# Performance work log

Hardware: AMD Instinct MI355X
Metric: run time of the kernel (lower is better)

## Reference

```python
import jax, jax.numpy as jnp
import numpy as np

B, T, C, H = 4, 2048, 1024, 16
HD = C // H  # head_size = 64


def setup_inputs() -> dict:
    key = jax.random.key(0)
    ks = jax.random.split(key, 8)
    s = 0.02
    return {
        "k": jax.random.normal(ks[0], (B, T, C), jnp.float32),
        "q": jax.random.normal(ks[1], (B, T, C), jnp.float32),
        "v": jax.random.normal(ks[2], (B, T, C), jnp.float32),
        "mask": jnp.ones((B, T, T), dtype=bool),
        "Wk": jax.random.normal(ks[3], (C, C), jnp.float32) * s,
        "bk": jnp.zeros((C,), jnp.float32),
        "Wq": jax.random.normal(ks[4], (C, C), jnp.float32) * s,
        "bq": jnp.zeros((C,), jnp.float32),
        "Wv": jax.random.normal(ks[5], (C, C), jnp.float32) * s,
        "bv": jnp.zeros((C,), jnp.float32),
        "Wo": jax.random.normal(ks[6], (C, C), jnp.float32) * s,
        "bo": jnp.zeros((C,), jnp.float32),
    }


def reference(k, q, v, mask, Wk, bk, Wq, bq, Wv, bv, Wo, bo):
    Bn, Tk, Cn = k.shape
    Tq = q.shape[1]
    hd = Cn // H
    # linear projections
    kp = (k @ Wk + bk).reshape(Bn, Tk, H, hd).transpose(0, 2, 1, 3)  # (B,H,Tk,hd)
    qp = (q @ Wq + bq).reshape(Bn, Tq, H, hd).transpose(0, 2, 1, 3)  # (B,H,Tq,hd)
    vp = (v @ Wv + bv).reshape(Bn, Tk, H, hd).transpose(0, 2, 1, 3)  # (B,H,Tk,hd)
    # scaled scores (B,H,Tq,Tk)
    att = jnp.einsum("bhqd,bhkd->bhqk", qp, kp) * (1.0 / jnp.sqrt(jnp.float32(hd)))
    # combined causal + padding mask
    causal = jnp.tril(jnp.ones((Tq, Tk), dtype=bool))  # (Tq,Tk)
    m = causal[None, None, :, :] & mask[:, None, :, :]  # (B,H|1,Tq,Tk)
    att = jnp.where(m, att, jnp.float32(-1e9))
    att = jax.nn.softmax(att, axis=-1)
    # dropout p=0.0 -> identity
    y = jnp.einsum("bhqk,bhkd->bhqd", att, vp)  # (B,H,Tq,hd)
    y = y.transpose(0, 2, 1, 3).reshape(Bn, Tq, Cn)
    return y @ Wo + bo
```

## Files before the change

### kernel.cpp

```cpp
#include <hip/hip_runtime.h>


#define BATCH 4
#define T_SEQ 2048
#define C_DIM 1024
#define NH 16
#define HD 64

typedef _Float16 f16;
typedef __attribute__((ext_vector_type(4))) _Float16 half4;
typedef __attribute__((ext_vector_type(8))) _Float16 half8;
typedef __attribute__((ext_vector_type(4))) float f32x4;

__device__ inline void gld_lds16(const f16* g, f16* l) {
    __builtin_amdgcn_global_load_lds(
        (const __attribute__((address_space(1))) void*)g,
        (__attribute__((address_space(3))) void*)l, 16, 0, 0);
}

__device__ inline void prep_tile(const float* __restrict__ src, f16* __restrict__ dst)
{
    __shared__ __align__(16) f16 Tl[64][72];
    const int tid = threadIdx.x;
    const int k0 = blockIdx.x * 64, n0 = blockIdx.y * 64;
#pragma unroll
    for (int p = 0; p < 4; ++p) {
        const int kr = p * 16 + (tid >> 4);
        const int nc = (tid & 15) * 4;
        float4 v = *(const float4*)(src + (size_t)(k0 + kr) * C_DIM + n0 + nc);
        Tl[nc + 0][kr] = (f16)v.x;
        Tl[nc + 1][kr] = (f16)v.y;
        Tl[nc + 2][kr] = (f16)v.z;
        Tl[nc + 3][kr] = (f16)v.w;
    }
    __syncthreads();
#pragma unroll
    for (int p = 0; p < 2; ++p) {
        const int nr = p * 32 + (tid >> 3);
        const int kc = (tid & 7) * 8;
        *(half8*)(dst + (size_t)(n0 + nr) * C_DIM + k0 + kc) = *(const half8*)&Tl[nr][kc];
    }
}

__global__ __launch_bounds__(256) void prep_weights(const float* __restrict__ src,
                                                    f16* __restrict__ dst)
{
    prep_tile(src, dst);
}

__global__ __launch_bounds__(256) void prep_weights3(const float* __restrict__ W0,
                                                     const float* __restrict__ W1,
                                                     const float* __restrict__ W2,
                                                     f16* __restrict__ D0,
                                                     f16* __restrict__ D1,
                                                     f16* __restrict__ D2)
{
    const int z = blockIdx.z;
    const float* src = (z == 0) ? W0 : (z == 1) ? W1 : W2;
    f16* dst = (z == 0) ? D0 : (z == 1) ? D1 : D2;
    prep_tile(src, dst);
}


__global__ __launch_bounds__(256) void qkv_gemm(const float* __restrict__ Xq,
                                                const float* __restrict__ Xk,
                                                const float* __restrict__ Xv,
                                                const f16* __restrict__ Wt3,
                                                const float* __restrict__ bqp,
                                                const float* __restrict__ bkp,
                                                const float* __restrict__ bvp,
                                                f16* __restrict__ Qp,
                                                f16* __restrict__ Kp,
                                                f16* __restrict__ Vc)
{
    __shared__ __align__(16) f16 As[2][128 * 40];
    __shared__ __align__(16) f16 Bs[2][128 * 32];

    const int g = blockIdx.x >> 6;
    const float* __restrict__ Xf   = (g == 0) ? Xq : (g == 1) ? Xk : Xv;
    const float* __restrict__ bias = (g == 0) ? bqp : (g == 1) ? bkp : bvp;
    const f16* __restrict__ Wt     = Wt3 + (size_t)g * C_DIM * C_DIM;
    f16* __restrict__ outH         = (g == 0) ? Qp : (g == 1) ? Kp : Vc;

    const int tid  = threadIdx.x;
    const int m0   = (blockIdx.x & 63) * 128;
    const int n0   = blockIdx.y * 128;
    const int lane = tid & 63;
    const int wv   = tid >> 6;
    const int wm   = (wv >> 1) * 64;
    const int wn   = (wv & 1) * 64;
    const int l15  = lane & 15;
    const int quad = lane >> 4;
    const int xg   = (quad ^ ((l15 >> 1) & 3)) << 3;
    const int cSwz = ((lane & 3) ^ ((lane >> 3) & 3)) << 3;
    const int ar   = tid / 8;
    const int ac4  = (tid & 7) * 4;
    const int brow = (wv * 2) * 16 + (lane >> 2);

    f32x4 acc[4][4];
#pragma unroll
    for (int i = 0; i < 4; i++)
#pragma unroll
        for (int j = 0; j < 4; j++) acc[i][j] = (f32x4){0.f, 0.f, 0.f, 0.f};

#pragma unroll
    for (int i = 0; i < 4; i++) {
        float4 v = *(const float4*)(Xf + (size_t)(m0 + ar + i * 32) * C_DIM + ac4);
        half4 h;
        h[0] = (f16)v.x; h[1] = (f16)v.y; h[2] = (f16)v.z; h[3] = (f16)v.w;
        *(half4*)&As[0][(ar + i * 32) * 40 + ac4] = h;
    }
#pragma unroll
    for (int i = 0; i < 2; ++i) {
        const int seg = wv * 2 + i;
        gld_lds16(Wt + (size_t)(n0 + brow + i * 16) * C_DIM + cSwz, &Bs[0][seg * 512]);
    }
    __syncthreads();

    for (int kt = 0; kt < 32; ++kt) {
        const int cur = kt & 1, nxt = cur ^ 1;
        const int kk  = (kt + 1) * 32;

        float4 av[4];
        if (kt < 31) {
#pragma unroll
            for (int i = 0; i < 4; i++)
                av[i] = *(const float4*)(Xf + (size_t)(m0 + ar + i * 32) * C_DIM + kk + ac4);
#pragma unroll
            for (int i = 0; i < 2; ++i) {
                const int seg = wv * 2 + i;
                gld_lds16(Wt + (size_t)(n0 + brow + i * 16) * C_DIM + kk + cSwz,
                          &Bs[nxt][seg * 512]);
            }
        }

        half8 af[4], bf[4];
#pragma unroll
        for (int t = 0; t < 4; t++) af[t] = *(const half8*)&As[cur][(wm + t * 16 + l15) * 40 + quad * 8];
#pragma unroll
        for (int t = 0; t < 4; t++) bf[t] = *(const half8*)&Bs[cur][(wn + t * 16 + l15) * 32 + xg];
#pragma unroll
        for (int tm = 0; tm < 4; tm++)
#pragma unroll
            for (int tn = 0; tn < 4; tn++)
                acc[tm][tn] = __builtin_amdgcn_mfma_f32_16x16x32_f16(af[tm], bf[tn], acc[tm][tn], 0, 0, 0);

        if (kt < 31) {
#pragma unroll
            for (int i = 0; i < 4; i++) {
                half4 h;
                h[0] = (f16)av[i].x; h[1] = (f16)av[i].y;
                h[2] = (f16)av[i].z; h[3] = (f16)av[i].w;
                *(half4*)&As[nxt][(ar + i * 32) * 40 + ac4] = h;
            }
        }
        __syncthreads();
    }

#pragma unroll
    for (int tm = 0; tm < 4; tm++) {
        const int gmb = m0 + wm + tm * 16 + quad * 4;
#pragma unroll
        for (int tn = 0; tn < 4; tn++) {
            const int gn = n0 + wn + tn * 16 + l15;
            const float bv = bias[gn];
            const int h = gn >> 6;
            const int d = gn & 63;
#pragma unroll
            for (int r = 0; r < 4; r++) {
                const int row = gmb + r;
                const float val = acc[tm][tn][r] + bv;
                const int b = row >> 11;
                const int t = row & (T_SEQ - 1);
                const size_t hb = ((size_t)(b * NH + h)) * T_SEQ * HD;
                if (g == 0) {
                    outH[hb + (size_t)t * HD + d] = (f16)(val * 0.18033688f);
                } else if (g == 1) {
                    outH[hb + (size_t)t * HD + ((((d >> 3) + t) & 7) << 3) + (d & 7)] = (f16)val;
                } else {
                    outH[hb + (size_t)(t >> 6) * 4096 + d * 64 +
                         ((((t >> 3) + d) & 7) << 3) + (t & 7)] = (f16)val;
                }
            }
        }
    }
}

__global__ __launch_bounds__(256) void gemm_out(const f16* __restrict__ Xh,
                                                const f16* __restrict__ Wt,
                                                const float* __restrict__ bias,
                                                float* __restrict__ outF)
{
    __shared__ __align__(16) f16 As[2][128 * 32];
    __shared__ __align__(16) f16 Bs[2][128 * 32];

    const int tid  = threadIdx.x;
    const int m0   = blockIdx.x * 128;
    const int n0   = blockIdx.y * 128;
    const int lane = tid & 63;
    const int wv   = tid >> 6;
    const int wm   = (wv >> 1) * 64;
    const int wn   = (wv & 1) * 64;
    const int l15  = lane & 15;
    const int quad = lane >> 4;
    const int xg   = (quad ^ ((l15 >> 1) & 3)) << 3;
    const int cSwz = ((lane & 3) ^ ((lane >> 3) & 3)) << 3;
    const int brow = (wv * 2) * 16 + (lane >> 2);

    f32x4 acc[4][4];
#pragma unroll
    for (int i = 0; i < 4; i++)
#pragma unroll
        for (int j = 0; j < 4; j++) acc[i][j] = (f32x4){0.f, 0.f, 0.f, 0.f};

#pragma unroll
    for (int i = 0; i < 2; ++i) {
        const int seg = wv * 2 + i;
        gld_lds16(Xh + (size_t)(m0 + brow + i * 16) * C_DIM + cSwz, &As[0][seg * 512]);
        gld_lds16(Wt + (size_t)(n0 + brow + i * 16) * C_DIM + cSwz, &Bs[0][seg * 512]);
    }
    __syncthreads();

    for (int kt = 0; kt < 32; ++kt) {
        const int cur = kt & 1, nxt = cur ^ 1;
        const int kk  = (kt + 1) * 32;

        if (kt < 31) {
#pragma unroll
            for (int i = 0; i < 2; ++i) {
                const int seg = wv * 2 + i;
                gld_lds16(Xh + (size_t)(m0 + brow + i * 16) * C_DIM + kk + cSwz, &As[nxt][seg * 512]);
                gld_lds16(Wt + (size_t)(n0 + brow + i * 16) * C_DIM + kk + cSwz, &Bs[nxt][seg * 512]);
            }
        }

        half8 af[4], bf[4];
#pragma unroll
        for (int t = 0; t < 4; t++) af[t] = *(const half8*)&As[cur][(wm + t * 16 + l15) * 32 + xg];
#pragma unroll
        for (int t = 0; t < 4; t++) bf[t] = *(const half8*)&Bs[cur][(wn + t * 16 + l15) * 32 + xg];
#pragma unroll
        for (int tm = 0; tm < 4; tm++)
#pragma unroll
            for (int tn = 0; tn < 4; tn++)
                acc[tm][tn] = __builtin_amdgcn_mfma_f32_16x16x32_f16(af[tm], bf[tn], acc[tm][tn], 0, 0, 0);
        __syncthreads();
    }

#pragma unroll
    for (int tm = 0; tm < 4; tm++) {
        const int gmb = m0 + wm + tm * 16 + quad * 4;
#pragma unroll
        for (int tn = 0; tn < 4; tn++) {
            const int gn = n0 + wn + tn * 16 + l15;
            const float bv = bias[gn];
#pragma unroll
            for (int r = 0; r < 4; r++)
                outF[(size_t)(gmb + r) * C_DIM + gn] = acc[tm][tn][r] + bv;
        }
    }
}

__global__ __launch_bounds__(256) void attn_kernel(const f16* __restrict__ Qp,
                                                   const f16* __restrict__ Kp,
                                                   const f16* __restrict__ Vc,
                                                   f16* __restrict__ Y)
{
    __shared__ __align__(16) f16 Ks[2][4096];
    __shared__ __align__(16) f16 Vs[2][4096];

    const int tid  = threadIdx.x;
    const int lane = tid & 63;
    const int wv   = tid >> 6;
    const int l15  = lane & 15;
    const int quad = lane >> 4;
    const int bh   = blockIdx.x & 63;
    const int ub   = blockIdx.x >> 6;
    const int u    = (ub << 2) | wv;
    int qT[2];
    qT[0] = 16 * u;
    qT[1] = 2032 - 16 * u;

    const f16* Qh = Qp + (size_t)bh * T_SEQ * HD;
    const f16* Kh = Kp + (size_t)bh * T_SEQ * HD;
    const f16* Vh = Vc + (size_t)bh * T_SEQ * HD;

    half8 aq[2][2];
#pragma unroll
    for (int m = 0; m < 2; m++)
#pragma unroll
        for (int kh = 0; kh < 2; kh++)
            aq[m][kh] = *(const half8*)(Qh + (size_t)(qT[m] + l15) * HD + kh * 32 + quad * 8);

    f32x4 o[2][4];
#pragma unroll
    for (int m = 0; m < 2; m++)
#pragma unroll
        for (int dt = 0; dt < 4; dt++) o[m][dt] = (f32x4){0.f, 0.f, 0.f, 0.f};
    float lsum[2] = {0.f, 0.f};

    const int nC0   = (16 * u + 79) >> 6;
    const int nC1   = (2111 - 16 * u) >> 6;
    const int nCblk = (2111 - 64 * ub) >> 6;

    auto stage = [&](int buf, int kc) {
        const f16* kg = Kh + (size_t)kc * 4096 + wv * 512;
        const f16* vg = Vh + (size_t)kc * 4096 + wv * 512;
        f16* kl = &Ks[buf][wv * 512];
        f16* vl = &Vs[buf][wv * 512];
        gld_lds16(kg + lane * 8, kl);
        gld_lds16(kg + 2048 + lane * 8, kl + 2048);
        gld_lds16(vg + lane * 8, vl);
        gld_lds16(vg + 2048 + lane * 8, vl + 2048);
    };

    stage(0, 0);
    __syncthreads();

    for (int kc = 0; kc < nCblk; ++kc) {
        const int cur = kc & 1;
        if (kc + 1 < nCblk) stage(cur ^ 1, kc + 1);

        if (kc < nC1) {
            const int k0 = kc * 64;
            const int mStart = (kc < nC0) ? 0 : 1;

            f32x4 st[2][4];
#pragma unroll
            for (int nt = 0; nt < 4; ++nt) {
                const f16* kr = &Ks[cur][(nt * 16 + l15) * 64];
                half8 bk0 = *(const half8*)(kr + (((quad + l15) & 7) << 3));
                half8 bk1 = *(const half8*)(kr + (((4 + quad + l15) & 7) << 3));
                {
                    f32x4 z = (f32x4){0.f, 0.f, 0.f, 0.f};
                    z = __builtin_amdgcn_mfma_f32_16x16x32_f16(bk0, aq[1][0], z, 0, 0, 0);
                    z = __builtin_amdgcn_mfma_f32_16x16x32_f16(bk1, aq[1][1], z, 0, 0, 0);
                    st[1][nt] = z;
                }
                if (mStart == 0) {
                    f32x4 z = (f32x4){0.f, 0.f, 0.f, 0.f};
                    z = __builtin_amdgcn_mfma_f32_16x16x32_f16(bk0, aq[0][0], z, 0, 0, 0);
                    z = __builtin_amdgcn_mfma_f32_16x16x32_f16(bk1, aq[0][1], z, 0, 0, 0);
                    st[0][nt] = z;
                }
            }

            half4 pf[2][4];
#pragma unroll
            for (int m = 0; m < 2; ++m) {
                if (m < mStart) continue;
                const bool needMask = (k0 + 63 > qT[m]);
                const int q = qT[m] + l15;
#pragma unroll
                for (int nt = 0; nt < 4; ++nt) {
#pragma unroll
                    for (int r = 0; r < 4; ++r) {
                        const int key = k0 + nt * 16 + quad * 4 + r;
                        float p = __builtin_exp2f(st[m][nt][r]);
                        if (needMask && key > q) p = 0.f;
                        lsum[m] += p;
                        pf[m][nt][r] = (f16)p;
                    }
                }
            }

#pragma unroll
            for (int nt = 0; nt < 4; ++nt) {
                const int c0 = nt * 2 + (quad >> 1);
#pragma unroll
                for (int dt = 0; dt < 4; ++dt) {
                    const int d = dt * 16 + l15;
                    half4 bv = *(const half4*)(&Vs[cur][d * 64 + (((c0 + d) & 7) << 3) + ((quad & 1) << 2)]);
                    o[1][dt] = __builtin_amdgcn_mfma_f32_16x16x16f16(pf[1][nt], bv, o[1][dt], 0, 0, 0);
                    if (mStart == 0)
                        o[0][dt] = __builtin_amdgcn_mfma_f32_16x16x16f16(pf[0][nt], bv, o[0][dt], 0, 0, 0);
                }
            }
        }
        __syncthreads();
    }

    const int b = bh >> 4;
    const int h = bh & 15;
#pragma unroll
    for (int m = 0; m < 2; m++) {
        float l = lsum[m];
        l += __shfl_xor(l, 16);
        l += __shfl_xor(l, 32);
#pragma unroll
        for (int r = 0; r < 4; r++) {
            const float lr  = __shfl(l, quad * 4 + r);
            const float inv = 1.0f / lr;
            const int qr = qT[m] + quad * 4 + r;
#pragma unroll
            for (int dt = 0; dt < 4; dt++)
                Y[((size_t)(b * T_SEQ + qr)) * C_DIM + h * HD + dt * 16 + l15] = (f16)(o[m][dt][r] * inv);
        }
    }
}

extern "C" void kernel_launch(void* const* d_in, const int* in_sizes, int n_in,
                              void* d_out, int out_size, void* d_ws, size_t ws_size,
                              hipStream_t stream)
{
    const float* k  = (const float*)d_in[0];
    const float* q  = (const float*)d_in[1];
    const float* v  = (const float*)d_in[2];
    const float* Wk = (const float*)d_in[4];
    const float* bk = (const float*)d_in[5];
    const float* Wq = (const float*)d_in[6];
    const float* bq = (const float*)d_in[7];
    const float* Wv = (const float*)d_in[8];
    const float* bv = (const float*)d_in[9];
    const float* Wo = (const float*)d_in[10];
    const float* bo = (const float*)d_in[11];
    float* out = (float*)d_out;

    const size_t E  = (size_t)BATCH * T_SEQ * C_DIM;
    const size_t WE = (size_t)C_DIM * C_DIM;

    f16* R0 = (f16*)d_ws;
    f16* R1 = R0 + E;
    f16* R2 = R1 + E;
    f16* R3 = R2 + E;

    f16* Kp  = R0;
    f16* Qp  = R1;
    f16* Vc  = R2;
    f16* Y   = R3;
    f16* WtQ = R3;
    f16* WtK = R3 + WE;
    f16* WtV = R3 + 2 * WE;
    f16* WtO = R1;

    dim3 blk(256);
    prep_weights3<<<dim3(16, 16, 3), blk, 0, stream>>>(Wq, Wk, Wv, WtQ, WtK, WtV);
    qkv_gemm<<<dim3(192, 8), blk, 0, stream>>>(q, k, v, WtQ, bq, bk, bv, Qp, Kp, Vc);
    attn_kernel<<<dim3(1024), blk, 0, stream>>>(Qp, Kp, Vc, Y);
    prep_weights<<<dim3(16, 16), blk, 0, stream>>>(Wo, WtO);
    gemm_out<<<dim3(64, 8), blk, 0, stream>>>(Y, WtO, bo, out);
}
```

Measured before the change: 418.3 us.

## Software-pipeline GEMM A-tile loads two steps ahead with explicit waitcnt barriers

Both the QKV projection GEMM and the output projection GEMM now prefetch the A operand into registers two k-steps ahead. The main loop is unrolled by two with ping-pong register buffers, and __syncthreads is replaced by hand-placed s_waitcnt vmcnt/lgkmcnt plus s_barrier and sched_barrier fences. In the output GEMM, the A tile moves from direct global-to-LDS loads to register loads followed by LDS stores. The aim is to hide global load latency behind the MFMA work and avoid waiting on all outstanding memory operations at each barrier. In exchange it adds register pressure and relies on hand-counted vmcnt values being correct.

```diff
diff --git a/kernel.cpp b/kernel.cpp
--- a/kernel.cpp
+++ b/kernel.cpp
@@ -60,7 +60,6 @@
     f16* dst = (z == 0) ? D0 : (z == 1) ? D1 : D2;
     prep_tile(src, dst);
 }
-
 
 __global__ __launch_bounds__(256) void qkv_gemm(const float* __restrict__ Xq,
                                                 const float* __restrict__ Xk,
@@ -111,50 +110,72 @@
         *(half4*)&As[0][(ar + i * 32) * 40 + ac4] = h;
     }
 #pragma unroll
-    for (int i = 0; i < 2; ++i) {
-        const int seg = wv * 2 + i;
-        gld_lds16(Wt + (size_t)(n0 + brow + i * 16) * C_DIM + cSwz, &Bs[0][seg * 512]);
-    }
-    __syncthreads();
-
-    for (int kt = 0; kt < 32; ++kt) {
-        const int cur = kt & 1, nxt = cur ^ 1;
-        const int kk  = (kt + 1) * 32;
-
-        float4 av[4];
-        if (kt < 31) {
-#pragma unroll
-            for (int i = 0; i < 4; i++)
-                av[i] = *(const float4*)(Xf + (size_t)(m0 + ar + i * 32) * C_DIM + kk + ac4);
-#pragma unroll
-            for (int i = 0; i < 2; ++i) {
-                const int seg = wv * 2 + i;
-                gld_lds16(Wt + (size_t)(n0 + brow + i * 16) * C_DIM + kk + cSwz,
-                          &Bs[nxt][seg * 512]);
-            }
-        }
-
+    for (int i = 0; i < 2; ++i)
+        gld_lds16(Wt + (size_t)(n0 + brow + i * 16) * C_DIM + cSwz, &Bs[0][(wv * 2 + i) * 512]);
+    __builtin_amdgcn_sched_barrier(0);
+    float4 avA[4], avB[4];
+#pragma unroll
+    for (int i = 0; i < 4; i++)
+        avA[i] = *(const float4*)(Xf + (size_t)(m0 + ar + i * 32) * C_DIM + 32 + ac4);
+    asm volatile("s_waitcnt vmcnt(4) lgkmcnt(0)" ::: "memory");
+    __builtin_amdgcn_sched_barrier(0);
+    __builtin_amdgcn_s_barrier();
+
+#define QKV_STEP(KT, CUR, NXT, AVC, AVN, VMEND)                                          \
+    {                                                                                    \
+        const int kk1 = ((KT) + 1) * 32;                                                 \
+        _Pragma("unroll")                                                                \
+        for (int i = 0; i < 2; ++i)                                                      \
+            gld_lds16(Wt + (size_t)(n0 + brow + i * 16) * C_DIM + kk1 + cSwz,            \
+                      &Bs[NXT][(wv * 2 + i) * 512]);                                     \
+        __builtin_amdgcn_sched_barrier(0);                           \
+        if ((KT) + 2 < 32) {                                                             \
+            const int kk2 = ((KT) + 2) * 32;                                             \
+            _Pragma("unroll")                                                            \
+            for (int i = 0; i < 4; i++)                                                  \
+                AVN[i] = *(const float4*)(Xf + (size_t)(m0 + ar + i * 32) * C_DIM + kk2 + ac4); \
+        }                                                                                \
+        half8 af[4], bf[4];                                                              \
+        _Pragma("unroll")                                                                \
+        for (int t = 0; t < 4; t++)                                                      \
+            af[t] = *(const half8*)&As[CUR][(wm + t * 16 + l15) * 40 + quad * 8];        \
+        _Pragma("unroll")                                                                \
+        for (int t = 0; t < 4; t++)                                                      \
+            bf[t] = *(const half8*)&Bs[CUR][(wn + t * 16 + l15) * 32 + xg];              \
+        _Pragma("unroll")                                                                \
+        for (int tm = 0; tm < 4; tm++)                                                   \
+            _Pragma("unroll")                                                            \
+            for (int tn = 0; tn < 4; tn++)                                               \
+                acc[tm][tn] = __builtin_amdgcn_mfma_f32_16x16x32_f16(af[tm], bf[tn], acc[tm][tn], 0, 0, 0); \
+        _Pragma("unroll")                                                                \
+        for (int i = 0; i < 4; i++) {                                                    \
+            half4 h;                                                                     \
+            h[0] = (f16)AVC[i].x; h[1] = (f16)AVC[i].y;                                  \
+            h[2] = (f16)AVC[i].z; h[3] = (f16)AVC[i].w;                                  \
+            *(half4*)&As[NXT][(ar + i * 32) * 40 + ac4] = h;                             \
+        }                                                                                \
+        asm volatile("s_waitcnt " VMEND " lgkmcnt(0)" ::: "memory");                     \
+        __builtin_amdgcn_sched_barrier(0);                                               \
+        __builtin_amdgcn_s_barrier();                                                    \
+    }
+
+    for (int kt = 0; kt < 30; kt += 2) {
+        QKV_STEP(kt,     0, 1, avA, avB, "vmcnt(4)");
+        QKV_STEP(kt + 1, 1, 0, avB, avA, "vmcnt(4)");
+    }
+    QKV_STEP(30, 0, 1, avA, avB, "vmcnt(0)");
+#undef QKV_STEP
+    {
         half8 af[4], bf[4];
 #pragma unroll
-        for (int t = 0; t < 4; t++) af[t] = *(const half8*)&As[cur][(wm + t * 16 + l15) * 40 + quad * 8];
-#pragma unroll
-        for (int t = 0; t < 4; t++) bf[t] = *(const half8*)&Bs[cur][(wn + t * 16 + l15) * 32 + xg];
+        for (int t = 0; t < 4; t++) af[t] = *(const half8*)&As[1][(wm + t * 16 + l15) * 40 + quad * 8];
+#pragma unroll
+        for (int t = 0; t < 4; t++) bf[t] = *(const half8*)&Bs[1][(wn + t * 16 + l15) * 32 + xg];
 #pragma unroll
         for (int tm = 0; tm < 4; tm++)
 #pragma unroll
             for (int tn = 0; tn < 4; tn++)
                 acc[tm][tn] = __builtin_amdgcn_mfma_f32_16x16x32_f16(af[tm], bf[tn], acc[tm][tn], 0, 0, 0);
-
-        if (kt < 31) {
-#pragma unroll
-            for (int i = 0; i < 4; i++) {
-                half4 h;
-                h[0] = (f16)av[i].x; h[1] = (f16)av[i].y;
-                h[2] = (f16)av[i].z; h[3] = (f16)av[i].w;
-                *(half4*)&As[nxt][(ar + i * 32) * 40 + ac4] = h;
-            }
-        }
-        __syncthreads();
     }
 
 #pragma unroll
@@ -215,36 +236,69 @@
 
 #pragma unroll
     for (int i = 0; i < 2; ++i) {
-        const int seg = wv * 2 + i;
-        gld_lds16(Xh + (size_t)(m0 + brow + i * 16) * C_DIM + cSwz, &As[0][seg * 512]);
-        gld_lds16(Wt + (size_t)(n0 + brow + i * 16) * C_DIM + cSwz, &Bs[0][seg * 512]);
-    }
-    __syncthreads();
-
-    for (int kt = 0; kt < 32; ++kt) {
-        const int cur = kt & 1, nxt = cur ^ 1;
-        const int kk  = (kt + 1) * 32;
-
-        if (kt < 31) {
-#pragma unroll
-            for (int i = 0; i < 2; ++i) {
-                const int seg = wv * 2 + i;
-                gld_lds16(Xh + (size_t)(m0 + brow + i * 16) * C_DIM + kk + cSwz, &As[nxt][seg * 512]);
-                gld_lds16(Wt + (size_t)(n0 + brow + i * 16) * C_DIM + kk + cSwz, &Bs[nxt][seg * 512]);
-            }
-        }
-
+        gld_lds16(Xh + (size_t)(m0 + brow + i * 16) * C_DIM + cSwz, &As[0][(wv * 2 + i) * 512]);
+        gld_lds16(Wt + (size_t)(n0 + brow + i * 16) * C_DIM + cSwz, &Bs[0][(wv * 2 + i) * 512]);
+    }
+    __builtin_amdgcn_sched_barrier(0);
+    half8 avA[2], avB[2];
+#pragma unroll
+    for (int i = 0; i < 2; ++i)
+        avA[i] = *(const half8*)(Xh + (size_t)(m0 + brow + i * 16) * C_DIM + 32 + cSwz);
+    asm volatile("s_waitcnt vmcnt(2) lgkmcnt(0)" ::: "memory");
+    __builtin_amdgcn_sched_barrier(0);
+    __builtin_amdgcn_s_barrier();
+
+#define OUT_STEP(KT, CUR, NXT, AVC, AVN, VMEND)                                          \
+    {                                                                                    \
+        const int kk1 = ((KT) + 1) * 32;                                                 \
+        _Pragma("unroll")                                                                \
+        for (int i = 0; i < 2; ++i)                                                      \
+            gld_lds16(Wt + (size_t)(n0 + brow + i * 16) * C_DIM + kk1 + cSwz,            \
+                      &Bs[NXT][(wv * 2 + i) * 512]);                                     \
+        __builtin_amdgcn_sched_barrier(0);                                               \
+        if ((KT) + 2 < 32) {                                                             \
+            const int kk2 = ((KT) + 2) * 32;                                             \
+            _Pragma("unroll")                                                            \
+            for (int i = 0; i < 2; ++i)                                                  \
+                AVN[i] = *(const half8*)(Xh + (size_t)(m0 + brow + i * 16) * C_DIM + kk2 + cSwz); \
+        }                                                                                \
+        half8 af[4], bf[4];                                                              \
+        _Pragma("unroll")                                                                \
+        for (int t = 0; t < 4; t++)                                                      \
+            af[t] = *(const half8*)&As[CUR][(wm + t * 16 + l15) * 32 + xg];              \
+        _Pragma("unroll")                                                                \
+        for (int t = 0; t < 4; t++)                                                      \
+            bf[t] = *(const half8*)&Bs[CUR][(wn + t * 16 + l15) * 32 + xg];              \
+        _Pragma("unroll")                                                                \
+        for (int tm = 0; tm < 4; tm++)                                                   \
+            _Pragma("unroll")                                                            \
+            for (int tn = 0; tn < 4; tn++)                                               \
+                acc[tm][tn] = __builtin_amdgcn_mfma_f32_16x16x32_f16(af[tm], bf[tn], acc[tm][tn], 0, 0, 0); \
+        _Pragma("unroll")                                                                \
+        for (int i = 0; i < 2; ++i)                                                      \
+            *(half8*)&As[NXT][(wv * 2 + i) * 512 + lane * 8] = AVC[i];                   \
+        asm volatile("s_waitcnt " VMEND " lgkmcnt(0)" ::: "memory");                     \
+        __builtin_amdgcn_sched_barrier(0);                                               \
+        __builtin_amdgcn_s_barrier();                                                    \
+    }
+
+    for (int kt = 0; kt < 30; kt += 2) {
+        OUT_STEP(kt,     0, 1, avA, avB, "vmcnt(2)");
+        OUT_STEP(kt + 1, 1, 0, avB, avA, "vmcnt(2)");
+    }
+    OUT_STEP(30, 0, 1, avA, avB, "vmcnt(0)");
+#undef OUT_STEP
+    {
         half8 af[4], bf[4];
 #pragma unroll
-        for (int t = 0; t < 4; t++) af[t] = *(const half8*)&As[cur][(wm + t * 16 + l15) * 32 + xg];
-#pragma unroll
-        for (int t = 0; t < 4; t++) bf[t] = *(const half8*)&Bs[cur][(wn + t * 16 + l15) * 32 + xg];
+        for (int t = 0; t < 4; t++) af[t] = *(const half8*)&As[1][(wm + t * 16 + l15) * 32 + xg];
+#pragma unroll
+        for (int t = 0; t < 4; t++) bf[t] = *(const half8*)&Bs[1][(wn + t * 16 + l15) * 32 + xg];
 #pragma unroll
         for (int tm = 0; tm < 4; tm++)
 #pragma unroll
             for (int tn = 0; tn < 4; tn++)
                 acc[tm][tn] = __builtin_amdgcn_mfma_f32_16x16x32_f16(af[tm], bf[tn], acc[tm][tn], 0, 0, 0);
-        __syncthreads();
     }
 
 #pragma unroll
```

Result: slower. 437.0 us (+4.5%).

## Deepen QKV GEMM prefetch to two stages with explicit waitcnt scheduling

Applied to the files above, without the earlier changes.

The QKV projection GEMM now prefetches two k-tiles ahead. The fp32 activations are held in two rotating register sets and the fp16 weights in a triple-buffered LDS ring. The loop is unrolled by two, and __syncthreads is replaced with manual s_waitcnt vmcnt counts, sched_barriers and s_barrier, so global loads stay in flight across iterations. This is meant to hide global-memory latency better, at the cost of more LDS and registers and of fragile hand-counted wait values.

```diff
diff --git a/kernel.cpp b/kernel.cpp
--- a/kernel.cpp
+++ b/kernel.cpp
@@ -60,7 +60,6 @@
     f16* dst = (z == 0) ? D0 : (z == 1) ? D1 : D2;
     prep_tile(src, dst);
 }
-
 
 __global__ __launch_bounds__(256) void qkv_gemm(const float* __restrict__ Xq,
                                                 const float* __restrict__ Xk,
@@ -74,7 +73,7 @@
                                                 f16* __restrict__ Vc)
 {
     __shared__ __align__(16) f16 As[2][128 * 40];
-    __shared__ __align__(16) f16 Bs[2][128 * 32];
+    __shared__ __align__(16) f16 Bs[3][128 * 32];
 
     const int g = blockIdx.x >> 6;
     const float* __restrict__ Xf   = (g == 0) ? Xq : (g == 1) ? Xk : Xv;
@@ -103,58 +102,112 @@
 #pragma unroll
         for (int j = 0; j < 4; j++) acc[i][j] = (f32x4){0.f, 0.f, 0.f, 0.f};
 
+    float4 rA[4], rB[4];
+
+#pragma unroll
+    for (int i = 0; i < 4; i++)
+        rA[i] = *(const float4*)(Xf + (size_t)(m0 + ar + i * 32) * C_DIM + ac4);
+#pragma unroll
+    for (int i = 0; i < 2; ++i)
+        gld_lds16(Wt + (size_t)(n0 + brow + i * 16) * C_DIM + cSwz, &Bs[0][(wv * 2 + i) * 512]);
+#pragma unroll
+    for (int i = 0; i < 4; i++)
+        rB[i] = *(const float4*)(Xf + (size_t)(m0 + ar + i * 32) * C_DIM + 32 + ac4);
+#pragma unroll
+    for (int i = 0; i < 2; ++i)
+        gld_lds16(Wt + (size_t)(n0 + brow + i * 16) * C_DIM + 32 + cSwz, &Bs[1][(wv * 2 + i) * 512]);
+    __builtin_amdgcn_sched_barrier(0);
+    asm volatile("s_waitcnt vmcnt(8)" ::: "memory");
+    __builtin_amdgcn_sched_barrier(0);
 #pragma unroll
     for (int i = 0; i < 4; i++) {
-        float4 v = *(const float4*)(Xf + (size_t)(m0 + ar + i * 32) * C_DIM + ac4);
         half4 h;
-        h[0] = (f16)v.x; h[1] = (f16)v.y; h[2] = (f16)v.z; h[3] = (f16)v.w;
+        h[0] = (f16)rA[i].x; h[1] = (f16)rA[i].y; h[2] = (f16)rA[i].z; h[3] = (f16)rA[i].w;
         *(half4*)&As[0][(ar + i * 32) * 40 + ac4] = h;
     }
-#pragma unroll
-    for (int i = 0; i < 2; ++i) {
-        const int seg = wv * 2 + i;
-        gld_lds16(Wt + (size_t)(n0 + brow + i * 16) * C_DIM + cSwz, &Bs[0][seg * 512]);
-    }
-    __syncthreads();
-
-    for (int kt = 0; kt < 32; ++kt) {
-        const int cur = kt & 1, nxt = cur ^ 1;
-        const int kk  = (kt + 1) * 32;
-
-        float4 av[4];
-        if (kt < 31) {
-#pragma unroll
-            for (int i = 0; i < 4; i++)
-                av[i] = *(const float4*)(Xf + (size_t)(m0 + ar + i * 32) * C_DIM + kk + ac4);
-#pragma unroll
-            for (int i = 0; i < 2; ++i) {
-                const int seg = wv * 2 + i;
-                gld_lds16(Wt + (size_t)(n0 + brow + i * 16) * C_DIM + kk + cSwz,
-                          &Bs[nxt][seg * 512]);
-            }
-        }
-
+    asm volatile("s_waitcnt vmcnt(6) lgkmcnt(0)" ::: "memory");
+    __builtin_amdgcn_sched_barrier(0);
+    __builtin_amdgcn_s_barrier();
+
+#define QKV_STEP(KT, RLOAD, RWRITE)                                                      \
+    {                                                                                    \
+        const int cur = (KT) & 1, nxt = cur ^ 1;                                         \
+        const int bc  = (KT) % 3, bn = ((KT) + 2) % 3;                                   \
+        const int kk2 = ((KT) + 2) * 32;                                                 \
+        _Pragma("unroll")                                                                \
+        for (int i = 0; i < 4; i++)                                                      \
+            RLOAD[i] = *(const float4*)(Xf + (size_t)(m0 + ar + i * 32) * C_DIM + kk2 + ac4); \
+        _Pragma("unroll")                                                                \
+        for (int i = 0; i < 2; ++i)                                                      \
+            gld_lds16(Wt + (size_t)(n0 + brow + i * 16) * C_DIM + kk2 + cSwz,            \
+                      &Bs[bn][(wv * 2 + i) * 512]);                                      \
+        __builtin_amdgcn_sched_barrier(0);                                               \
+        half8 af[4], bf[4];                                                              \
+        _Pragma("unroll")                                                                \
+        for (int t = 0; t < 4; t++)                                                      \
+            af[t] = *(const half8*)&As[cur][(wm + t * 16 + l15) * 40 + quad * 8];        \
+        _Pragma("unroll")                                                                \
+        for (int t = 0; t < 4; t++)                                                      \
+            bf[t] = *(const half8*)&Bs[bc][(wn + t * 16 + l15) * 32 + xg];               \
+        _Pragma("unroll")                                                                \
+        for (int tm = 0; tm < 4; tm++)                                                   \
+            _Pragma("unroll")                                                            \
+            for (int tn = 0; tn < 4; tn++)                                               \
+                acc[tm][tn] = __builtin_amdgcn_mfma_f32_16x16x32_f16(af[tm], bf[tn], acc[tm][tn], 0, 0, 0); \
+        asm volatile("s_waitcnt vmcnt(8)" ::: "memory");               \
+        __builtin_amdgcn_sched_barrier(0);                                               \
+        _Pragma("unroll")                                                                \
+        for (int i = 0; i < 4; i++) {                                                    \
+            half4 h;                                                                     \
+            h[0] = (f16)RWRITE[i].x; h[1] = (f16)RWRITE[i].y;                            \
+            h[2] = (f16)RWRITE[i].z; h[3] = (f16)RWRITE[i].w;                            \
+            *(half4*)&As[nxt][(ar + i * 32) * 40 + ac4] = h;                             \
+        }                                                                                \
+        asm volatile("s_waitcnt vmcnt(6) lgkmcnt(0)" ::: "memory");    \
+        __builtin_amdgcn_sched_barrier(0);                                               \
+        __builtin_amdgcn_s_barrier();                                                    \
+    }
+
+    for (int kt = 0; kt < 30; kt += 2) {
+        QKV_STEP(kt,     rA, rB);
+        QKV_STEP(kt + 1, rB, rA);
+    }
+#undef QKV_STEP
+
+    {
         half8 af[4], bf[4];
 #pragma unroll
-        for (int t = 0; t < 4; t++) af[t] = *(const half8*)&As[cur][(wm + t * 16 + l15) * 40 + quad * 8];
-#pragma unroll
-        for (int t = 0; t < 4; t++) bf[t] = *(const half8*)&Bs[cur][(wn + t * 16 + l15) * 32 + xg];
+        for (int t = 0; t < 4; t++) af[t] = *(const half8*)&As[0][(wm + t * 16 + l15) * 40 + quad * 8];
+#pragma unroll
+        for (int t = 0; t < 4; t++) bf[t] = *(const half8*)&Bs[0][(wn + t * 16 + l15) * 32 + xg];
 #pragma unroll
         for (int tm = 0; tm < 4; tm++)
 #pragma unroll
             for (int tn = 0; tn < 4; tn++)
                 acc[tm][tn] = __builtin_amdgcn_mfma_f32_16x16x32_f16(af[tm], bf[tn], acc[tm][tn], 0, 0, 0);
-
-        if (kt < 31) {
-#pragma unroll
-            for (int i = 0; i < 4; i++) {
-                half4 h;
-                h[0] = (f16)av[i].x; h[1] = (f16)av[i].y;
-                h[2] = (f16)av[i].z; h[3] = (f16)av[i].w;
-                *(half4*)&As[nxt][(ar + i * 32) * 40 + ac4] = h;
-            }
-        }
-        __syncthreads();
+        asm volatile("s_waitcnt vmcnt(2)" ::: "memory");
+        __builtin_amdgcn_sched_barrier(0);
+#pragma unroll
+        for (int i = 0; i < 4; i++) {
+            half4 h;
+            h[0] = (f16)rB[i].x; h[1] = (f16)rB[i].y; h[2] = (f16)rB[i].z; h[3] = (f16)rB[i].w;
+            *(half4*)&As[1][(ar + i * 32) * 40 + ac4] = h;
+        }
+        asm volatile("s_waitcnt vmcnt(0) lgkmcnt(0)" ::: "memory");
+        __builtin_amdgcn_sched_barrier(0);
+        __builtin_amdgcn_s_barrier();
+    }
+    {
+        half8 af[4], bf[4];
+#pragma unroll
+        for (int t = 0; t < 4; t++) af[t] = *(const half8*)&As[1][(wm + t * 16 + l15) * 40 + quad * 8];
+#pragma unroll
+        for (int t = 0; t < 4; t++) bf[t] = *(const half8*)&Bs[1][(wn + t * 16 + l15) * 32 + xg];
+#pragma unroll
+        for (int tm = 0; tm < 4; tm++)
+#pragma unroll
+            for (int tn = 0; tn < 4; tn++)
+                acc[tm][tn] = __builtin_amdgcn_mfma_f32_16x16x32_f16(af[tm], bf[tn], acc[tm][tn], 0, 0, 0);
     }
 
 #pragma unroll
@@ -215,9 +268,8 @@
 
 #pragma unroll
     for (int i = 0; i < 2; ++i) {
-        const int seg = wv * 2 + i;
-        gld_lds16(Xh + (size_t)(m0 + brow + i * 16) * C_DIM + cSwz, &As[0][seg * 512]);
-        gld_lds16(Wt + (size_t)(n0 + brow + i * 16) * C_DIM + cSwz, &Bs[0][seg * 512]);
+        gld_lds16(Xh + (size_t)(m0 + brow + i * 16) * C_DIM + cSwz, &As[0][(wv * 2 + i) * 512]);
+        gld_lds16(Wt + (size_t)(n0 + brow + i * 16) * C_DIM + cSwz, &Bs[0][(wv * 2 + i) * 512]);
     }
     __syncthreads();
 
@@ -228,9 +280,8 @@
         if (kt < 31) {
 #pragma unroll
             for (int i = 0; i < 2; ++i) {
-                const int seg = wv * 2 + i;
-                gld_lds16(Xh + (size_t)(m0 + brow + i * 16) * C_DIM + kk + cSwz, &As[nxt][seg * 512]);
-                gld_lds16(Wt + (size_t)(n0 + brow + i * 16) * C_DIM + kk + cSwz, &Bs[nxt][seg * 512]);
+                gld_lds16(Xh + (size_t)(m0 + brow + i * 16) * C_DIM + kk + cSwz, &As[nxt][(wv * 2 + i) * 512]);
+                gld_lds16(Wt + (size_t)(n0 + brow + i * 16) * C_DIM + kk + cSwz, &Bs[nxt][(wv * 2 + i) * 512]);
             }
         }
 
```

New measurement: 429.6 us. +2.7%, slower.
